# Optimization experiments

Hardware: AMD Instinct MI355X
Metric: run time of the kernel (lower is better)

Reference implementation:

```python
import jax, jax.numpy as jnp
import numpy as np

N = 20000
E = 320000
IN_DIM = 128
HIDDEN = 256
HEADS = 4
HD = HIDDEN // HEADS  # 64 per-head channels in layer 1
OUT_DIM = 128
NEG_SLOPE = 0.2
BN_EPS = 1e-5


def setup_inputs() -> dict:
    key = jax.random.key(0)
    ks = jax.random.split(key, 16)
    inp = {
        "x": jax.random.normal(ks[0], (N, IN_DIM), dtype=jnp.float32),
        "edge_index": jax.random.randint(ks[1], (2, E), 0, N, dtype=jnp.int64),
        # layer 1: GATConv(IN_DIM, HD, heads=HEADS, concat=True)
        "W1": jax.random.normal(ks[2], (IN_DIM, HEADS * HD), dtype=jnp.float32) * (1.0 / np.sqrt(IN_DIM)),
        "att_src1": jax.random.normal(ks[3], (HEADS, HD), dtype=jnp.float32) * 0.1,
        "att_dst1": jax.random.normal(ks[4], (HEADS, HD), dtype=jnp.float32) * 0.1,
        "bias1": jnp.zeros((HEADS * HD,), dtype=jnp.float32),
        "bn1_gamma": jnp.ones((HIDDEN,), dtype=jnp.float32),
        "bn1_beta": jnp.zeros((HIDDEN,), dtype=jnp.float32),
        # layer 2: GATConv(HIDDEN, OUT_DIM, heads=1, concat=False)
        "W2": jax.random.normal(ks[5], (HIDDEN, OUT_DIM), dtype=jnp.float32) * (1.0 / np.sqrt(HIDDEN)),
        "att_src2": jax.random.normal(ks[6], (1, OUT_DIM), dtype=jnp.float32) * 0.1,
        "att_dst2": jax.random.normal(ks[7], (1, OUT_DIM), dtype=jnp.float32) * 0.1,
        "bias2": jnp.zeros((OUT_DIM,), dtype=jnp.float32),
        "bn2_gamma": jnp.ones((OUT_DIM,), dtype=jnp.float32),
        "bn2_beta": jnp.zeros((OUT_DIM,), dtype=jnp.float32),
    }
    return inp


def _gat_conv(x, src, dst, W, a_src, a_dst, bias, heads, concat):
    """PyG GATConv with add_self_loops=True (self-loops already in src/dst)."""
    n = x.shape[0]
    hd = W.shape[1] // heads
    h = (x @ W).reshape(n, heads, hd)                     # [N, H, hd]
    alpha_s = jnp.einsum('nhd,hd->nh', h, a_src)          # [N, H]
    alpha_d = jnp.einsum('nhd,hd->nh', h, a_dst)          # [N, H]
    e = alpha_s[src] + alpha_d[dst]                       # [Etot, H]
    e = jnp.where(e > 0, e, NEG_SLOPE * e)                # leaky_relu
    # edge-softmax over incoming edges of each destination node
    m = jax.ops.segment_max(e, dst, num_segments=n)       # [N, H]
    ex = jnp.exp(e - m[dst])
    denom = jax.ops.segment_sum(ex, dst, num_segments=n)  # [N, H]
    alpha = ex / (denom[dst] + 1e-16)                     # [Etot, H]
    msg = h[src] * alpha[..., None]                       # [Etot, H, hd]
    out = jax.ops.segment_sum(msg, dst, num_segments=n)   # [N, H, hd]
    if concat:
        out = out.reshape(n, heads * hd)
    else:
        out = out.mean(axis=1)
    return out + bias


def _batch_norm(x, gamma, beta):
    mean = x.mean(axis=0)
    var = ((x - mean) ** 2).mean(axis=0)  # biased, training-mode BN
    return (x - mean) * jax.lax.rsqrt(var + BN_EPS) * gamma + beta


def reference(x, edge_index, W1, att_src1, att_dst1, bias1, bn1_gamma, bn1_beta,
              W2, att_src2, att_dst2, bias2, bn2_gamma, bn2_beta):
    n = x.shape[0]
    loop = jnp.arange(n, dtype=edge_index.dtype)
    src = jnp.concatenate([edge_index[0], loop])  # add self-loops (PyG default)
    dst = jnp.concatenate([edge_index[1], loop])

    h = _gat_conv(x, src, dst, W1, att_src1, att_dst1, bias1, HEADS, True)
    h = _batch_norm(h, bn1_gamma, bn1_beta)
    h = jax.nn.elu(h)

    h = _gat_conv(h, src, dst, W2, att_src2, att_dst2, bias2, 1, False)
    h = _batch_norm(h, bn2_gamma, bn2_beta)
    return h
```

## Files before the change

kernel.cpp:

```cpp
#include <hip/hip_runtime.h>
#include <type_traits>

constexpr int N_N  = 20000;
constexpr int N_E  = 320000;
constexpr int N_ET = N_E + N_N;
constexpr int IN_D = 128;
constexpr int HID  = 256;
constexpr int H1   = 4;
constexpr int OUTD = 128;
constexpr float SLOPE = 0.2f;
constexpr float BNEPS = 1e-5f;
constexpr int NPART = 32;

typedef unsigned short u16;
typedef float f32x4 __attribute__((ext_vector_type(4)));
typedef short bf16x8 __attribute__((ext_vector_type(8)));

__device__ __forceinline__ float bf2f(u16 u) { return __uint_as_float((unsigned)u << 16); }
__device__ __forceinline__ u16 f2bf(float f) {
  unsigned u = __float_as_uint(f);
  unsigned r = u + 0x7FFFu + ((u >> 16) & 1u);
  return (u16)(r >> 16);
}

__global__ __launch_bounds__(256) void prep_k(const int* __restrict__ ei,
                                              const float* __restrict__ W1,
                                              const float* __restrict__ W2,
                                              u16* __restrict__ wp1,
                                              u16* __restrict__ wp2,
                                              int* __restrict__ cnt) {
  const int i = blockIdx.x * 256 + threadIdx.x;
  if (i < IN_D * HID) {
    const int n = i >> 7, k = i & 127;
    wp1[i] = f2bf(W1[(size_t)k * HID + n]);
  }
  if (i < HID * OUTD) {
    const int n = i >> 8, k = i & 255;
    wp2[i] = f2bf(W2[(size_t)k * OUTD + n]);
  }
  if (i < N_ET) {
    const int dst = (i < N_E) ? ei[N_E + i] : (i - N_E);
    atomicAdd(&cnt[dst], 1);
  }
}

__global__ __launch_bounds__(1024) void scan_k(const int* __restrict__ cnt,
                                               int* __restrict__ rowptr,
                                               int* __restrict__ wcur) {
  __shared__ int wsum[17];
  const int tid = threadIdx.x, lane = tid & 63, wv = tid >> 6;
  constexpr int CHK = 20;
  const int base = tid * CHK;
  int c[CHK];
  int s = 0;
#pragma unroll
  for (int j = 0; j < CHK; ++j) {
    const int idx = base + j;
    c[j] = (idx < N_N) ? cnt[idx] : 0;
    s += c[j];
  }
  const int own = s;
#pragma unroll
  for (int off = 1; off < 64; off <<= 1) {
    const int v = __shfl_up(s, off, 64);
    if (lane >= off) s += v;
  }
  if (lane == 63) wsum[wv] = s;
  __syncthreads();
  if (tid == 0) {
    int run = 0;
#pragma unroll
    for (int i = 0; i < 16; ++i) { const int t = wsum[i]; wsum[i] = run; run += t; }
    wsum[16] = run;
  }
  __syncthreads();
  int run = wsum[wv] + (s - own);
#pragma unroll
  for (int j = 0; j < CHK; ++j) {
    const int idx = base + j;
    if (idx < N_N) {
      rowptr[idx] = run;
      wcur[idx]   = run;
      run += c[j];
    }
  }
  if (tid == 0) rowptr[N_N] = wsum[16];
}

constexpr int GB1 = N_N / 16;
__global__ __launch_bounds__(256) void sg_k(const float* __restrict__ x,
                                            const u16* __restrict__ wp,
                                            const float* __restrict__ asrc,
                                            const float* __restrict__ adst,
                                            u16* __restrict__ h,
                                            float* __restrict__ as_,
                                            float* __restrict__ ad_,
                                            const int* __restrict__ ei,
                                            int* __restrict__ wcur,
                                            int* __restrict__ col) {
  const int tid = threadIdx.x;
  if (blockIdx.x >= GB1) {
    const int i = (blockIdx.x - GB1) * 256 + tid;
    if (i >= N_ET) return;
    int s, dst;
    if (i < N_E) { s = ei[i]; dst = ei[N_E + i]; } else { s = dst = i - N_E; }
    const int pos = atomicAdd(&wcur[dst], 1);
    col[pos] = s;
    return;
  }
  const int wv = tid >> 6, lane = tid & 63;
  const int q = lane >> 4, t = lane & 15;
  const int m0 = blockIdx.x * 16;
  const int n0 = wv * 64;
  f32x4 acc[4] = {};
#pragma unroll
  for (int kb = 0; kb < 4; ++kb) {
    const int k0 = kb * 32 + q * 8;
    const float4 x0 = *(const float4*)(x + (size_t)(m0 + t) * 128 + k0);
    const float4 x1 = *(const float4*)(x + (size_t)(m0 + t) * 128 + k0 + 4);
    bf16x8 a;
    a[0] = (short)f2bf(x0.x); a[1] = (short)f2bf(x0.y);
    a[2] = (short)f2bf(x0.z); a[3] = (short)f2bf(x0.w);
    a[4] = (short)f2bf(x1.x); a[5] = (short)f2bf(x1.y);
    a[6] = (short)f2bf(x1.z); a[7] = (short)f2bf(x1.w);
#pragma unroll
    for (int nt = 0; nt < 4; ++nt) {
      const int n = n0 + nt * 16 + t;
      const bf16x8 b = *(const bf16x8*)(wp + (size_t)n * 128 + k0);
      acc[nt] = __builtin_amdgcn_mfma_f32_16x16x32_bf16(a, b, acc[nt], 0, 0, 0);
    }
  }
  float ps[4] = {0.f, 0.f, 0.f, 0.f}, pd[4] = {0.f, 0.f, 0.f, 0.f};
#pragma unroll
  for (int nt = 0; nt < 4; ++nt) {
    const int coln = n0 + nt * 16 + t;
    const float a_s = asrc[coln], a_d = adst[coln];
#pragma unroll
    for (int r = 0; r < 4; ++r) {
      const float d = acc[nt][r];
      h[(size_t)(m0 + q * 4 + r) * 256 + coln] = f2bf(d);
      ps[r] += d * a_s;
      pd[r] += d * a_d;
    }
  }
#pragma unroll
  for (int off = 1; off < 16; off <<= 1)
#pragma unroll
    for (int r = 0; r < 4; ++r) {
      ps[r] += __shfl_xor(ps[r], off, 64);
      pd[r] += __shfl_xor(pd[r], off, 64);
    }
  if (t == 0) {
#pragma unroll
    for (int r = 0; r < 4; ++r) {
      const int row = m0 + q * 4 + r;
      as_[(size_t)row * 4 + wv] = ps[r];
      ad_[(size_t)row * 4 + wv] = pd[r];
    }
  }
}

__global__ __launch_bounds__(256) void gat_agg1_k(const int* __restrict__ rowptr,
                                                  const int* __restrict__ col,
                                                  const u16* __restrict__ h,
                                                  const float* __restrict__ as_,
                                                  const float* __restrict__ ad_,
                                                  u16* __restrict__ out,
                                                  float* __restrict__ accp) {
  __shared__ int   s_s[4][64];
  __shared__ float s_w[4][64][2];
  __shared__ float st_s[2][256], st_q[2][256];
  const int tid = threadIdx.x;
  const int wv = tid >> 6, lane = tid & 63;
  const int nl = wv >> 1, half = wv & 1;
  const int n = blockIdx.x * 2 + nl;
  const int beg = rowptr[n], end = rowptr[n + 1];
  const int c0 = half * 128 + lane * 2;
  const int hl = lane >> 5;
  const int hb = half * 2;
  const float adv0 = ad_[n * 4 + hb], adv1 = ad_[n * 4 + hb + 1];

  float a0 = 0.f, a1 = 0.f, smh = 0.f;

  for (int j0 = beg; j0 < end; j0 += 64) {
    const int cnt = min(64, end - j0);
    const int j = j0 + lane;
    const int sl = col[(j < end) ? j : beg];
    s_s[wv][lane] = sl;
    const float4 av = *(const float4*)(as_ + (size_t)sl * 4);
    const float* ap = (const float*)&av;
    float e0 = ap[hb] + adv0;     e0 = e0 > 0.f ? e0 : SLOPE * e0;
    float e1 = ap[hb + 1] + adv1; e1 = e1 > 0.f ? e1 : SLOPE * e1;
    s_w[wv][lane][0] = (j < end) ? __expf(e0) : 0.f;
    s_w[wv][lane][1] = (j < end) ? __expf(e1) : 0.f;

    int jj = 0;
    for (; jj + 8 <= cnt; jj += 8) {
      int sv[8]; float wt[8]; ushort2 g[8];
#pragma unroll
      for (int u = 0; u < 8; ++u) {
        sv[u] = s_s[wv][jj + u];
        wt[u] = s_w[wv][jj + u][hl];
      }
#pragma unroll
      for (int u = 0; u < 8; ++u) g[u] = *(const ushort2*)(h + (size_t)sv[u] * 256 + c0);
#pragma unroll
      for (int u = 0; u < 8; ++u) {
        smh += wt[u];
        a0 = fmaf(wt[u], bf2f(g[u].x), a0);
        a1 = fmaf(wt[u], bf2f(g[u].y), a1);
      }
    }
    for (; jj < cnt; ++jj) {
      const int s = s_s[wv][jj];
      const float w = s_w[wv][jj][hl];
      const ushort2 g = *(const ushort2*)(h + (size_t)s * 256 + c0);
      smh += w;
      a0 = fmaf(w, bf2f(g.x), a0);
      a1 = fmaf(w, bf2f(g.y), a1);
    }
  }

  const float r = 1.f / (smh + 1e-16f);
  const float v0 = a0 * r, v1 = a1 * r;
  ushort2 o; o.x = f2bf(v0); o.y = f2bf(v1);
  *(ushort2*)(out + (size_t)n * 256 + c0) = o;

  st_s[nl][c0] = v0;     st_s[nl][c0 + 1] = v1;
  st_q[nl][c0] = v0 * v0; st_q[nl][c0 + 1] = v1 * v1;
  __syncthreads();
  {
    const int c = tid;
    const float s = st_s[0][c] + st_s[1][c];
    const float q = st_q[0][c] + st_q[1][c];
    float* dst = accp + (size_t)(blockIdx.x & (NPART - 1)) * 512;
    atomicAdd(&dst[c], s);
    atomicAdd(&dst[256 + c], q);
  }
}

__global__ __launch_bounds__(256) void gat_agg2_k(const int* __restrict__ rowptr,
                                                  const int* __restrict__ col,
                                                  const u16* __restrict__ h,
                                                  const float* __restrict__ as_,
                                                  const float* __restrict__ ad_,
                                                  u16* __restrict__ out,
                                                  float* __restrict__ accp) {
  __shared__ int   s_s[4][64];
  __shared__ float s_w[4][64];
  __shared__ float st_s[4][128], st_q[4][128];
  const int tid = threadIdx.x;
  const int wv = tid >> 6, lane = tid & 63;
  const int n = blockIdx.x * 4 + wv;
  const int beg = rowptr[n], end = rowptr[n + 1];
  const int c0 = lane * 2;
  const float adv = ad_[n];

  float a0 = 0.f, a1 = 0.f, smh = 0.f;

  for (int j0 = beg; j0 < end; j0 += 64) {
    const int cnt = min(64, end - j0);
    const int j = j0 + lane;
    const int sl = col[(j < end) ? j : beg];
    s_s[wv][lane] = sl;
    float e = as_[sl] + adv;
    e = e > 0.f ? e : SLOPE * e;
    s_w[wv][lane] = (j < end) ? __expf(e) : 0.f;

    int jj = 0;
    for (; jj + 8 <= cnt; jj += 8) {
      int sv[8]; float wt[8]; ushort2 g[8];
#pragma unroll
      for (int u = 0; u < 8; ++u) {
        sv[u] = s_s[wv][jj + u];
        wt[u] = s_w[wv][jj + u];
      }
#pragma unroll
      for (int u = 0; u < 8; ++u) g[u] = *(const ushort2*)(h + (size_t)sv[u] * 128 + c0);
#pragma unroll
      for (int u = 0; u < 8; ++u) {
        smh += wt[u];
        a0 = fmaf(wt[u], bf2f(g[u].x), a0);
        a1 = fmaf(wt[u], bf2f(g[u].y), a1);
      }
    }
    for (; jj < cnt; ++jj) {
      const int s = s_s[wv][jj];
      const float w = s_w[wv][jj];
      const ushort2 g = *(const ushort2*)(h + (size_t)s * 128 + c0);
      smh += w;
      a0 = fmaf(w, bf2f(g.x), a0);
      a1 = fmaf(w, bf2f(g.y), a1);
    }
  }

  const float r = 1.f / (smh + 1e-16f);
  const float v0 = a0 * r, v1 = a1 * r;
  ushort2 o; o.x = f2bf(v0); o.y = f2bf(v1);
  *(ushort2*)(out + (size_t)n * 128 + c0) = o;

  st_s[wv][c0] = v0;      st_s[wv][c0 + 1] = v1;
  st_q[wv][c0] = v0 * v0; st_q[wv][c0 + 1] = v1 * v1;
  __syncthreads();
  if (tid < 128) {
    const int c = tid;
    const float s = st_s[0][c] + st_s[1][c] + st_s[2][c] + st_s[3][c];
    const float q = st_q[0][c] + st_q[1][c] + st_q[2][c] + st_q[3][c];
    float* dst = accp + (size_t)(blockIdx.x & (NPART - 1)) * 256;
    atomicAdd(&dst[c], s);
    atomicAdd(&dst[128 + c], q);
  }
}

__global__ __launch_bounds__(256) void gemm2_mfma_k(const u16* __restrict__ hin,
                                                    const float* __restrict__ accp,
                                                    const float* __restrict__ g1,
                                                    const float* __restrict__ b1,
                                                    const u16* __restrict__ wp,
                                                    const float* __restrict__ asrc,
                                                    const float* __restrict__ adst,
                                                    u16* __restrict__ h2,
                                                    float* __restrict__ as_,
                                                    float* __restrict__ ad_) {
  __shared__ float scsh[512];
  __shared__ float red[2][32][2];
  const int tid = threadIdx.x;
  {
    float s = 0.f, q = 0.f;
#pragma unroll
    for (int p = 0; p < NPART; ++p) {
      s += accp[(size_t)p * 512 + tid];
      q += accp[(size_t)p * 512 + 256 + tid];
    }
    const float mean = s * (1.f / N_N);
    const float var  = q * (1.f / N_N) - mean * mean;
    const float inv  = rsqrtf(var + BNEPS);
    const float sc   = g1[tid] * inv;
    scsh[tid]       = sc;
    scsh[256 + tid] = b1[tid] - mean * sc;
  }
  __syncthreads();
  const int wv = tid >> 6, lane = tid & 63;
  const int q = lane >> 4, t = lane & 15;
  const int mh = wv >> 1, nh = wv & 1;
  const int m0 = blockIdx.x * 32 + mh * 16;
  const int n0 = nh * 64;
  f32x4 acc[4] = {};
#pragma unroll
  for (int kb = 0; kb < 8; ++kb) {
    const int k0 = kb * 32 + q * 8;
    const ushort4 u0 = *(const ushort4*)(hin + (size_t)(m0 + t) * 256 + k0);
    const ushort4 u1 = *(const ushort4*)(hin + (size_t)(m0 + t) * 256 + k0 + 4);
    const float4 sc0 = *(const float4*)(scsh + k0);
    const float4 sc1 = *(const float4*)(scsh + k0 + 4);
    const float4 sh0 = *(const float4*)(scsh + 256 + k0);
    const float4 sh1 = *(const float4*)(scsh + 256 + k0 + 4);
    float v[8];
    v[0] = bf2f(u0.x) * sc0.x + sh0.x;
    v[1] = bf2f(u0.y) * sc0.y + sh0.y;
    v[2] = bf2f(u0.z) * sc0.z + sh0.z;
    v[3] = bf2f(u0.w) * sc0.w + sh0.w;
    v[4] = bf2f(u1.x) * sc1.x + sh1.x;
    v[5] = bf2f(u1.y) * sc1.y + sh1.y;
    v[6] = bf2f(u1.z) * sc1.z + sh1.z;
    v[7] = bf2f(u1.w) * sc1.w + sh1.w;
    bf16x8 a;
#pragma unroll
    for (int j = 0; j < 8; ++j) {
      const float e = v[j] > 0.f ? v[j] : __expf(v[j]) - 1.f;
      a[j] = (short)f2bf(e);
    }
#pragma unroll
    for (int nt = 0; nt < 4; ++nt) {
      const int n = n0 + nt * 16 + t;
      const bf16x8 b = *(const bf16x8*)(wp + (size_t)n * 256 + k0);
      acc[nt] = __builtin_amdgcn_mfma_f32_16x16x32_bf16(a, b, acc[nt], 0, 0, 0);
    }
  }
  float ps[4] = {0.f, 0.f, 0.f, 0.f}, pd[4] = {0.f, 0.f, 0.f, 0.f};
#pragma unroll
  for (int nt = 0; nt < 4; ++nt) {
    const int coln = n0 + nt * 16 + t;
    const float a_s = asrc[coln], a_d = adst[coln];
#pragma unroll
    for (int r = 0; r < 4; ++r) {
      const float d = acc[nt][r];
      h2[(size_t)(m0 + q * 4 + r) * 128 + coln] = f2bf(d);
      ps[r] += d * a_s;
      pd[r] += d * a_d;
    }
  }
#pragma unroll
  for (int off = 1; off < 16; off <<= 1)
#pragma unroll
    for (int r = 0; r < 4; ++r) {
      ps[r] += __shfl_xor(ps[r], off, 64);
      pd[r] += __shfl_xor(pd[r], off, 64);
    }
  if (t == 0) {
#pragma unroll
    for (int r = 0; r < 4; ++r) {
      red[0][mh * 16 + q * 4 + r][nh] = ps[r];
      red[1][mh * 16 + q * 4 + r][nh] = pd[r];
    }
  }
  __syncthreads();
  if (tid < 32) {
    as_[(size_t)blockIdx.x * 32 + tid] = red[0][tid][0] + red[0][tid][1];
    ad_[(size_t)blockIdx.x * 32 + tid] = red[1][tid][0] + red[1][tid][1];
  }
}

__global__ __launch_bounds__(256) void apply_k(const u16* __restrict__ X,
                                               const float* __restrict__ accp,
                                               const float* __restrict__ gamma,
                                               const float* __restrict__ beta,
                                               float* __restrict__ Y) {
  __shared__ float s_sc[128], s_sh[128];
  const int tid = threadIdx.x;
  if (tid < 128) {
    float s = 0.f, q = 0.f;
#pragma unroll
    for (int p = 0; p < NPART; ++p) {
      s += accp[(size_t)p * 256 + tid];
      q += accp[(size_t)p * 256 + 128 + tid];
    }
    const float mean = s * (1.f / N_N);
    const float var  = q * (1.f / N_N) - mean * mean;
    const float inv  = rsqrtf(var + BNEPS);
    const float sc   = gamma[tid] * inv;
    s_sc[tid] = sc;
    s_sh[tid] = beta[tid] - mean * sc;
  }
  __syncthreads();
  constexpr size_t TOT = (size_t)N_N * OUTD;
  for (size_t i = ((size_t)blockIdx.x * 256 + tid) * 4; i < TOT;
       i += (size_t)gridDim.x * 256 * 4) {
    const ushort4 u = *(const ushort4*)(X + i);
    const int c = (int)(i & 127);
    float4 o;
    o.x = bf2f(u.x) * s_sc[c]     + s_sh[c];
    o.y = bf2f(u.y) * s_sc[c + 1] + s_sh[c + 1];
    o.z = bf2f(u.z) * s_sc[c + 2] + s_sh[c + 2];
    o.w = bf2f(u.w) * s_sc[c + 3] + s_sh[c + 3];
    *(float4*)(Y + i) = o;
  }
}

constexpr size_t OFF_WP1  = 0;
constexpr size_t OFF_WP2  = OFF_WP1  + (size_t)IN_D * HID / 2;
constexpr size_t OFF_H1   = OFF_WP2  + (size_t)HID * OUTD / 2;
constexpr size_t OFF_OUT1 = OFF_H1   + (size_t)N_N * HID / 2;
constexpr size_t OFF_H2   = OFF_OUT1 + (size_t)N_N * HID / 2;
constexpr size_t OFF_OUT2 = OFF_H2   + (size_t)N_N * OUTD / 2;
constexpr size_t OFF_AS1  = OFF_OUT2 + (size_t)N_N * OUTD / 2;
constexpr size_t OFF_AD1  = OFF_AS1  + (size_t)N_N * H1;
constexpr size_t OFF_AS2  = OFF_AD1  + (size_t)N_N * H1;
constexpr size_t OFF_AD2  = OFF_AS2  + (size_t)N_N;
constexpr size_t OFF_ROWP = OFF_AD2  + (size_t)N_N;
constexpr size_t OFF_COL  = OFF_ROWP + (size_t)(N_N + 1);
constexpr size_t OFF_WCUR = OFF_COL  + (size_t)N_ET;
constexpr size_t OFF_CNT  = OFF_WCUR + (size_t)N_N;
constexpr size_t OFF_ACC1 = OFF_CNT  + (size_t)N_N;
constexpr size_t OFF_ACC2 = OFF_ACC1 + (size_t)NPART * 512;
constexpr size_t OFF_ZEND = OFF_ACC2 + (size_t)NPART * 256;

extern "C" void kernel_launch(void* const* d_in, const int* in_sizes, int n_in,
                              void* d_out, int out_size, void* d_ws, size_t ws_size,
                              hipStream_t stream) {
  const float* x      = (const float*)d_in[0];
  const int*   ei     = (const int*)d_in[1];
  const float* W1     = (const float*)d_in[2];
  const float* asrc1  = (const float*)d_in[3];
  const float* adst1  = (const float*)d_in[4];
  const float* g1     = (const float*)d_in[6];
  const float* b1     = (const float*)d_in[7];
  const float* W2     = (const float*)d_in[8];
  const float* asrc2  = (const float*)d_in[9];
  const float* adst2  = (const float*)d_in[10];
  const float* g2     = (const float*)d_in[12];
  const float* b2     = (const float*)d_in[13];

  float* ws = (float*)d_ws;
  u16*   wp1   = (u16*)(ws + OFF_WP1);
  u16*   wp2   = (u16*)(ws + OFF_WP2);
  u16*   h1    = (u16*)(ws + OFF_H1);
  u16*   out1  = (u16*)(ws + OFF_OUT1);
  u16*   h2    = (u16*)(ws + OFF_H2);
  u16*   out2  = (u16*)(ws + OFF_OUT2);
  float* as1   = ws + OFF_AS1;
  float* ad1   = ws + OFF_AD1;
  float* as2   = ws + OFF_AS2;
  float* ad2   = ws + OFF_AD2;
  int*   rowp  = (int*)(ws + OFF_ROWP);
  int*   col   = (int*)(ws + OFF_COL);
  int*   wcur  = (int*)(ws + OFF_WCUR);
  int*   cnt   = (int*)(ws + OFF_CNT);
  float* acc1p = ws + OFF_ACC1;
  float* acc2p = ws + OFF_ACC2;
  float* outf  = (float*)d_out;

  hipMemsetAsync(cnt, 0, (OFF_ZEND - OFF_CNT) * sizeof(float), stream);

  const int eb = (N_ET + 255) / 256;
  prep_k<<<eb, 256, 0, stream>>>(ei, W1, W2, wp1, wp2, cnt);
  scan_k<<<1, 1024, 0, stream>>>(cnt, rowp, wcur);
  sg_k<<<GB1 + eb, 256, 0, stream>>>(x, wp1, asrc1, adst1, h1, as1, ad1, ei, wcur, col);
  gat_agg1_k<<<N_N / 2, 256, 0, stream>>>(rowp, col, h1, as1, ad1, out1, acc1p);
  gemm2_mfma_k<<<N_N / 32, 256, 0, stream>>>(out1, acc1p, g1, b1, wp2, asrc2, adst2, h2, as2, ad2);
  gat_agg2_k<<<N_N / 4, 256, 0, stream>>>(rowp, col, h2, as2, ad2, out2, acc2p);
  apply_k<<<512, 256, 0, stream>>>(out2, acc2p, g2, b2, outf);
}
```

Measured before the change: 257.5 us.

## Widen per-lane gathers and software-pipeline neighbor loads in GAT aggregation kernels

```diff
diff --git a/kernel.cpp b/kernel.cpp
--- a/kernel.cpp
+++ b/kernel.cpp
@@ -167,72 +167,87 @@
                                                   const float* __restrict__ ad_,
                                                   u16* __restrict__ out,
                                                   float* __restrict__ accp) {
-  __shared__ int   s_s[4][64];
-  __shared__ float s_w[4][64][2];
-  __shared__ float st_s[2][256], st_q[2][256];
+  __shared__ __align__(16) float s_w[4][64][4];
+  __shared__ __align__(16) float st_s[4][256], st_q[4][256];
   const int tid = threadIdx.x;
   const int wv = tid >> 6, lane = tid & 63;
-  const int nl = wv >> 1, half = wv & 1;
-  const int n = blockIdx.x * 2 + nl;
+  const int n = blockIdx.x * 4 + wv;
   const int beg = rowptr[n], end = rowptr[n + 1];
-  const int c0 = half * 128 + lane * 2;
-  const int hl = lane >> 5;
-  const int hb = half * 2;
-  const float adv0 = ad_[n * 4 + hb], adv1 = ad_[n * 4 + hb + 1];
-
-  float a0 = 0.f, a1 = 0.f, smh = 0.f;
+  const int c0 = lane * 4;
+  const int hl = lane >> 4;
+  const float4 adv = *(const float4*)(ad_ + (size_t)n * 4);
+
+  float a0 = 0.f, a1 = 0.f, a2 = 0.f, a3 = 0.f, smh = 0.f;
 
   for (int j0 = beg; j0 < end; j0 += 64) {
     const int cnt = min(64, end - j0);
     const int j = j0 + lane;
     const int sl = col[(j < end) ? j : beg];
-    s_s[wv][lane] = sl;
+
+    ushort4 gA[8];
+#pragma unroll
+    for (int u = 0; u < 8; ++u) {
+      const int sv = __shfl(sl, u, 64);
+      gA[u] = *(const ushort4*)(h + (size_t)sv * 256 + c0);
+    }
+
     const float4 av = *(const float4*)(as_ + (size_t)sl * 4);
-    const float* ap = (const float*)&av;
-    float e0 = ap[hb] + adv0;     e0 = e0 > 0.f ? e0 : SLOPE * e0;
-    float e1 = ap[hb + 1] + adv1; e1 = e1 > 0.f ? e1 : SLOPE * e1;
-    s_w[wv][lane][0] = (j < end) ? __expf(e0) : 0.f;
-    s_w[wv][lane][1] = (j < end) ? __expf(e1) : 0.f;
-
-    int jj = 0;
-    for (; jj + 8 <= cnt; jj += 8) {
-      int sv[8]; float wt[8]; ushort2 g[8];
+    float e0 = av.x + adv.x; e0 = e0 > 0.f ? e0 : SLOPE * e0;
+    float e1 = av.y + adv.y; e1 = e1 > 0.f ? e1 : SLOPE * e1;
+    float e2 = av.z + adv.z; e2 = e2 > 0.f ? e2 : SLOPE * e2;
+    float e3 = av.w + adv.w; e3 = e3 > 0.f ? e3 : SLOPE * e3;
+    const bool valid = j < end;
+    float4 w4;
+    w4.x = valid ? __expf(e0) : 0.f;
+    w4.y = valid ? __expf(e1) : 0.f;
+    w4.z = valid ? __expf(e2) : 0.f;
+    w4.w = valid ? __expf(e3) : 0.f;
+    *(float4*)(&s_w[wv][lane][0]) = w4;
+
+    const int rounds = (cnt + 7) >> 3;
+    for (int r = 0; r < rounds; ++r) {
+      ushort4 gB[8];
+      if (r + 1 < rounds) {
+        const int nb = (r + 1) * 8;
+#pragma unroll
+        for (int u = 0; u < 8; ++u) {
+          const int sv = __shfl(sl, nb + u, 64);
+          gB[u] = *(const ushort4*)(h + (size_t)sv * 256 + c0);
+        }
+      }
+      const int rb = r * 8;
 #pragma unroll
       for (int u = 0; u < 8; ++u) {
-        sv[u] = s_s[wv][jj + u];
-        wt[u] = s_w[wv][jj + u][hl];
+        const float w = s_w[wv][rb + u][hl];
+        smh += w;
+        a0 = fmaf(w, bf2f(gA[u].x), a0);
+        a1 = fmaf(w, bf2f(gA[u].y), a1);
+        a2 = fmaf(w, bf2f(gA[u].z), a2);
+        a3 = fmaf(w, bf2f(gA[u].w), a3);
       }
-#pragma unroll
-      for (int u = 0; u < 8; ++u) g[u] = *(const ushort2*)(h + (size_t)sv[u] * 256 + c0);
-#pragma unroll
-      for (int u = 0; u < 8; ++u) {
-        smh += wt[u];
-        a0 = fmaf(wt[u], bf2f(g[u].x), a0);
-        a1 = fmaf(wt[u], bf2f(g[u].y), a1);
+      if (r + 1 < rounds) {
+#pragma unroll
+        for (int u = 0; u < 8; ++u) gA[u] = gB[u];
       }
     }
-    for (; jj < cnt; ++jj) {
-      const int s = s_s[wv][jj];
-      const float w = s_w[wv][jj][hl];
-      const ushort2 g = *(const ushort2*)(h + (size_t)s * 256 + c0);
-      smh += w;
-      a0 = fmaf(w, bf2f(g.x), a0);
-      a1 = fmaf(w, bf2f(g.y), a1);
-    }
-  }
-
-  const float r = 1.f / (smh + 1e-16f);
-  const float v0 = a0 * r, v1 = a1 * r;
-  ushort2 o; o.x = f2bf(v0); o.y = f2bf(v1);
-  *(ushort2*)(out + (size_t)n * 256 + c0) = o;
-
-  st_s[nl][c0] = v0;     st_s[nl][c0 + 1] = v1;
-  st_q[nl][c0] = v0 * v0; st_q[nl][c0 + 1] = v1 * v1;
+  }
+
+  const float rr = 1.f / (smh + 1e-16f);
+  const float v0 = a0 * rr, v1 = a1 * rr, v2 = a2 * rr, v3 = a3 * rr;
+  ushort4 o;
+  o.x = f2bf(v0); o.y = f2bf(v1); o.z = f2bf(v2); o.w = f2bf(v3);
+  *(ushort4*)(out + (size_t)n * 256 + c0) = o;
+
+  float4 sv4, qv4;
+  sv4.x = v0; sv4.y = v1; sv4.z = v2; sv4.w = v3;
+  qv4.x = v0 * v0; qv4.y = v1 * v1; qv4.z = v2 * v2; qv4.w = v3 * v3;
+  *(float4*)(&st_s[wv][c0]) = sv4;
+  *(float4*)(&st_q[wv][c0]) = qv4;
   __syncthreads();
   {
     const int c = tid;
-    const float s = st_s[0][c] + st_s[1][c];
-    const float q = st_q[0][c] + st_q[1][c];
+    const float s = st_s[0][c] + st_s[1][c] + st_s[2][c] + st_s[3][c];
+    const float q = st_q[0][c] + st_q[1][c] + st_q[2][c] + st_q[3][c];
     float* dst = accp + (size_t)(blockIdx.x & (NPART - 1)) * 512;
     atomicAdd(&dst[c], s);
     atomicAdd(&dst[256 + c], q);
@@ -246,61 +261,79 @@
                                                   const float* __restrict__ ad_,
                                                   u16* __restrict__ out,
                                                   float* __restrict__ accp) {
-  __shared__ int   s_s[4][64];
-  __shared__ float s_w[4][64];
-  __shared__ float st_s[4][128], st_q[4][128];
+  __shared__ __align__(16) float st_s[4][128], st_q[4][128];
   const int tid = threadIdx.x;
   const int wv = tid >> 6, lane = tid & 63;
   const int n = blockIdx.x * 4 + wv;
   const int beg = rowptr[n], end = rowptr[n + 1];
-  const int c0 = lane * 2;
+  const int eh = lane >> 5;
+  const int cl = (lane & 31) * 4;
   const float adv = ad_[n];
 
-  float a0 = 0.f, a1 = 0.f, smh = 0.f;
+  float a0 = 0.f, a1 = 0.f, a2 = 0.f, a3 = 0.f, smh = 0.f;
 
   for (int j0 = beg; j0 < end; j0 += 64) {
     const int cnt = min(64, end - j0);
     const int j = j0 + lane;
     const int sl = col[(j < end) ? j : beg];
-    s_s[wv][lane] = sl;
     float e = as_[sl] + adv;
     e = e > 0.f ? e : SLOPE * e;
-    s_w[wv][lane] = (j < end) ? __expf(e) : 0.f;
-
-    int jj = 0;
-    for (; jj + 8 <= cnt; jj += 8) {
-      int sv[8]; float wt[8]; ushort2 g[8];
+    const float ew = (j < end) ? __expf(e) : 0.f;
+
+    const int rounds = (cnt + 15) >> 4;
+    ushort4 gA[8];
+#pragma unroll
+    for (int u = 0; u < 8; ++u) {
+      const int es = u * 2 + eh;
+      const int sv = __shfl(sl, es, 64);
+      gA[u] = *(const ushort4*)(h + (size_t)sv * 128 + cl);
+    }
+    for (int r = 0; r < rounds; ++r) {
+      ushort4 gB[8];
+      if (r + 1 < rounds) {
+        const int nb = (r + 1) * 16;
+#pragma unroll
+        for (int u = 0; u < 8; ++u) {
+          const int es = nb + u * 2 + eh;
+          const int sv = __shfl(sl, es, 64);
+          gB[u] = *(const ushort4*)(h + (size_t)sv * 128 + cl);
+        }
+      }
+      const int rb = r * 16;
 #pragma unroll
       for (int u = 0; u < 8; ++u) {
-        sv[u] = s_s[wv][jj + u];
-        wt[u] = s_w[wv][jj + u];
+        const float w = __shfl(ew, rb + u * 2 + eh, 64);
+        smh += w;
+        a0 = fmaf(w, bf2f(gA[u].x), a0);
+        a1 = fmaf(w, bf2f(gA[u].y), a1);
+        a2 = fmaf(w, bf2f(gA[u].z), a2);
+        a3 = fmaf(w, bf2f(gA[u].w), a3);
       }
-#pragma unroll
-      for (int u = 0; u < 8; ++u) g[u] = *(const ushort2*)(h + (size_t)sv[u] * 128 + c0);
-#pragma unroll
-      for (int u = 0; u < 8; ++u) {
-        smh += wt[u];
-        a0 = fmaf(wt[u], bf2f(g[u].x), a0);
-        a1 = fmaf(wt[u], bf2f(g[u].y), a1);
+      if (r + 1 < rounds) {
+#pragma unroll
+        for (int u = 0; u < 8; ++u) gA[u] = gB[u];
       }
     }
-    for (; jj < cnt; ++jj) {
-      const int s = s_s[wv][jj];
-      const float w = s_w[wv][jj];
-      const ushort2 g = *(const ushort2*)(h + (size_t)s * 128 + c0);
-      smh += w;
-      a0 = fmaf(w, bf2f(g.x), a0);
-      a1 = fmaf(w, bf2f(g.y), a1);
-    }
-  }
-
-  const float r = 1.f / (smh + 1e-16f);
-  const float v0 = a0 * r, v1 = a1 * r;
-  ushort2 o; o.x = f2bf(v0); o.y = f2bf(v1);
-  *(ushort2*)(out + (size_t)n * 128 + c0) = o;
-
-  st_s[wv][c0] = v0;      st_s[wv][c0 + 1] = v1;
-  st_q[wv][c0] = v0 * v0; st_q[wv][c0 + 1] = v1 * v1;
+  }
+
+  a0 += __shfl_xor(a0, 32, 64);
+  a1 += __shfl_xor(a1, 32, 64);
+  a2 += __shfl_xor(a2, 32, 64);
+  a3 += __shfl_xor(a3, 32, 64);
+  smh += __shfl_xor(smh, 32, 64);
+
+  const float rr = 1.f / (smh + 1e-16f);
+  const float v0 = a0 * rr, v1 = a1 * rr, v2 = a2 * rr, v3 = a3 * rr;
+  if (lane < 32) {
+    ushort4 o;
+    o.x = f2bf(v0); o.y = f2bf(v1); o.z = f2bf(v2); o.w = f2bf(v3);
+    *(ushort4*)(out + (size_t)n * 128 + cl) = o;
+    float4 sv4, qv4;
+    sv4.x = v0; sv4.y = v1; sv4.z = v2; sv4.w = v3;
+    qv4.x = v0 * v0; qv4.y = v1 * v1; qv4.z = v2 * v2; qv4.w = v3 * v3;
+    *(float4*)(&st_s[wv][cl]) = sv4;
+    *(float4*)(&st_q[wv][cl]) = qv4;
+  }
   __syncthreads();
   if (tid < 128) {
     const int c = tid;
@@ -506,7 +539,7 @@
   prep_k<<<eb, 256, 0, stream>>>(ei, W1, W2, wp1, wp2, cnt);
   scan_k<<<1, 1024, 0, stream>>>(cnt, rowp, wcur);
   sg_k<<<GB1 + eb, 256, 0, stream>>>(x, wp1, asrc1, adst1, h1, as1, ad1, ei, wcur, col);
-  gat_agg1_k<<<N_N / 2, 256, 0, stream>>>(rowp, col, h1, as1, ad1, out1, acc1p);
+  gat_agg1_k<<<N_N / 4, 256, 0, stream>>>(rowp, col, h1, as1, ad1, out1, acc1p);
   gemm2_mfma_k<<<N_N / 32, 256, 0, stream>>>(out1, acc1p, g1, b1, wp2, asrc2, adst2, h2, as2, ad2);
   gat_agg2_k<<<N_N / 4, 256, 0, stream>>>(rowp, col, h2, as2, ad2, out2, acc2p);
   apply_k<<<512, 256, 0, stream>>>(out2, acc2p, g2, b2, outf);
```

After: 235.5 us. 1.09x faster.
